# Optimization experiments

Hardware: AMD Instinct MI355X
Metric: run time of the kernel (lower is better)

Reference implementation:

```python
import jax, jax.numpy as jnp
import numpy as np

T = 0.5  # temperature from __init__


def setup_inputs() -> dict:
    key = jax.random.key(0)
    k1, k2, k3 = jax.random.split(key, 3)
    n, d = 8192, 256
    findings_embeddings = jax.random.normal(k1, (n, d), dtype=jnp.float32)
    impression_embeddings = jax.random.normal(k2, (n, d), dtype=jnp.float32)
    chexpert_label = jax.random.randint(k3, (n,), 0, 14, dtype=jnp.int64)
    return {
        "findings_embeddings": findings_embeddings,
        "impression_embeddings": impression_embeddings,
        "chexpert_label": chexpert_label,
    }


def reference(findings_embeddings, impression_embeddings, chexpert_label):
    n = findings_embeddings.shape[0]
    # [n, n] similarity matrix scaled by temperature
    logits = jnp.matmul(findings_embeddings, impression_embeddings.T) / T
    # zero out entries where labels match, except the diagonal (i != j)
    eq = chexpert_label[:, None] == chexpert_label[None, :]
    off_diag_eq = eq & ~jnp.eye(n, dtype=bool)
    logits = jnp.where(off_diag_eq, 0.0, logits)
    # trace(log_softmax_row + log_softmax_col) without materializing two [n,n] copies:
    # diag(log_softmax(L, axis)) = diag(L) - logsumexp(L, axis)
    diag = jnp.diagonal(logits)
    lse_row = jax.nn.logsumexp(logits, axis=1)  # findings -> impression direction
    lse_col = jax.nn.logsumexp(logits, axis=0)  # impression -> findings direction
    loss = -jnp.sum((diag - lse_row) + (diag - lse_col)) / n
    return loss
```

## Files before the change

kernel.cpp:

```cpp
#include <hip/hip_runtime.h>
#include <hip/hip_bf16.h>

#define N 8192
#define D 256
#define NSLICE 16
#define BM 128
#define TROWS 2
#define CB 32
#define COLS_PER_SLICE (N / NSLICE)
#define NT (COLS_PER_SLICE / CB)
#define NRB (N / BM)
#define TILE_B (CB * D)

#define CSHIFT 160.0f
#define K2LOG2E 2.885390082f
#define LN2F 0.6931471805599453f

typedef __attribute__((ext_vector_type(4))) float f32x4;

__device__ inline float fast_exp2(float x) { return __builtin_amdgcn_exp2f(x); }
__device__ inline float fast_log2(float x) { return __builtin_amdgcn_logf(x); }

__device__ inline void gload_lds16(const void* g, void* l) {
    __builtin_amdgcn_global_load_lds(
        (const __attribute__((address_space(1))) void*)g,
        (__attribute__((address_space(3))) void*)l, 16, 0, 0);
}

__device__ inline unsigned int pack_fp8x4(float a, float b, float c, float d) {
    unsigned int p = __builtin_amdgcn_cvt_pk_fp8_f32(a, b, 0, 0);
    p = __builtin_amdgcn_cvt_pk_fp8_f32(c, d, (int)p, 1);
    return p;
}

__global__ void convert_fp8(const float* __restrict__ F, const float* __restrict__ Imp,
                            unsigned int* __restrict__ Fb8, unsigned int* __restrict__ Ib8) {
    const int i = blockIdx.x * blockDim.x + threadIdx.x;
    if (blockIdx.y == 0) {
        const float4 v0 = reinterpret_cast<const float4*>(F)[i * 2];
        const float4 v1 = reinterpret_cast<const float4*>(F)[i * 2 + 1];
        Fb8[i * 2] = pack_fp8x4(v0.x, v0.y, v0.z, v0.w);
        Fb8[i * 2 + 1] = pack_fp8x4(v1.x, v1.y, v1.z, v1.w);
    } else {
        const int lane = i & 63;
        const int ks = (i >> 6) & 7;
        const int g = i >> 9;
        const int col = g * 16 + (lane & 15);
        const int k0 = ks * 32 + (lane >> 4) * 8;
        const float* src = Imp + (size_t)col * D + k0;
        const float4 v0 = *reinterpret_cast<const float4*>(src);
        const float4 v1 = *reinterpret_cast<const float4*>(src + 4);
        Ib8[i * 2] = pack_fp8x4(v0.x, v0.y, v0.z, v0.w);
        Ib8[i * 2 + 1] = pack_fp8x4(v1.x, v1.y, v1.z, v1.w);
    }
}

__global__ void label_hist(const int* __restrict__ labels, int* __restrict__ counts) {
    __shared__ int c[16];
    if (threadIdx.x < 16) c[threadIdx.x] = 0;
    __syncthreads();
    for (int i = threadIdx.x; i < N; i += blockDim.x) atomicAdd(&c[labels[i]], 1);
    __syncthreads();
    if (threadIdx.x < 16) counts[threadIdx.x] = c[threadIdx.x];
}

__launch_bounds__(256, 4)
__global__ void tile_pass(const unsigned char* __restrict__ Fb8,
                          const unsigned char* __restrict__ Ib8,
                          const int* __restrict__ labels,
                          float* __restrict__ partials_row,
                          float* __restrict__ partials_col) {
    __shared__ __align__(16) unsigned char Bsh[3 * TILE_B];
    __shared__ float colacc[4][COLS_PER_SLICE];
    __shared__ int labs[COLS_PER_SLICE];

    const int tid = threadIdx.x;
    const int lane = tid & 63;
    const int wave = tid >> 6;
    const int rb = blockIdx.x;
    const int row0 = rb * BM + wave * (16 * TROWS);
    const int c0 = blockIdx.y * COLS_PER_SLICE;
    const int lrow = lane & 15;
    const int kgrp = lane >> 4;

#define STAGE(buf, ct)                                                          \
    {                                                                           \
        const unsigned char* tbase = Ib8 + (size_t)(c0 + (ct) * CB) * D;        \
        _Pragma("unroll")                                                       \
        for (int i = 0; i < 2; ++i) {                                           \
            const int chunk = wave * 2 + i;                                     \
            gload_lds16(tbase + chunk * 1024 + lane * 16,                       \
                        &Bsh[(buf) * TILE_B + chunk * 1024 + lane * 16]);       \
        }                                                                       \
    }

    STAGE(0, 0);
    STAGE(1, 1);

    for (int i = tid; i < COLS_PER_SLICE; i += 256) {
        labs[i] = labels[c0 + i];
        colacc[0][i] = 0.f; colacc[1][i] = 0.f; colacc[2][i] = 0.f; colacc[3][i] = 0.f;
    }

    long afrag[TROWS][8];
#pragma unroll
    for (int t = 0; t < TROWS; ++t) {
        const unsigned char* arow = Fb8 + (size_t)(row0 + t * 16 + lrow) * D;
#pragma unroll
        for (int ks = 0; ks < 8; ++ks)
            afrag[t][ks] = *reinterpret_cast<const long*>(arow + ks * 32 + kgrp * 8);
    }
#pragma unroll
    for (int t = 0; t < TROWS; ++t)
#pragma unroll
        for (int ks = 0; ks < 8; ++ks)
            asm volatile("" : "+v"(afrag[t][ks]));

    int labr[TROWS][4];
#pragma unroll
    for (int t = 0; t < TROWS; ++t) {
        const int base = row0 + t * 16 + kgrp * 4;
#pragma unroll
        for (int r = 0; r < 4; ++r) labr[t][r] = labels[base + r];
    }

    float s[TROWS][4];
#pragma unroll
    for (int t = 0; t < TROWS; ++t)
#pragma unroll
        for (int r = 0; r < 4; ++r) s[t][r] = 0.0f;

    asm volatile("s_waitcnt vmcnt(2) lgkmcnt(0)" ::: "memory");
    __builtin_amdgcn_s_barrier();

    int cbuf = 0, sbuf = 2;
    for (int ct = 0; ct < NT; ++ct) {
        if (ct + 2 < NT) STAGE(sbuf, ct + 2);

        __builtin_amdgcn_s_setprio(1);
#pragma unroll
        for (int u = 0; u < 2; ++u) {
            long bfrag[8];
#pragma unroll
            for (int ks = 0; ks < 8; ++ks)
                bfrag[ks] = *reinterpret_cast<const long*>(
                    &Bsh[cbuf * TILE_B + (u * 8 + ks) * 512 + lane * 8]);

            const int labc = labs[ct * CB + u * 16 + lrow];
            float colpart = 0.0f;
            f32x4 acc[TROWS];
#pragma unroll
            for (int t = 0; t < TROWS; ++t) acc[t] = f32x4{0.f, 0.f, 0.f, 0.f};
#pragma unroll
            for (int ks = 0; ks < 8; ++ks)
#pragma unroll
                for (int t = 0; t < TROWS; ++t)
                    acc[t] = __builtin_amdgcn_mfma_f32_16x16x32_fp8_fp8(
                        afrag[t][ks], bfrag[ks], acc[t], 0, 0, 0);

#pragma unroll
            for (int t = 0; t < TROWS; ++t) {
#pragma unroll
                for (int r = 0; r < 4; ++r) {
                    float arg = __builtin_fmaf(acc[t][r], K2LOG2E, -CSHIFT);
                    arg = (labr[t][r] == labc) ? -1000.0f : arg;
                    float e = fast_exp2(arg);
                    s[t][r] += e;
                    colpart += e;
                }
            }
            colpart += __shfl_xor(colpart, 16, 64);
            colpart += __shfl_xor(colpart, 32, 64);
            if (kgrp == 0)
                colacc[wave][ct * CB + u * 16 + lrow] += colpart;
        }
        __builtin_amdgcn_s_setprio(0);

        if (ct + 2 < NT) {
            asm volatile("s_waitcnt vmcnt(2)" ::: "memory");
        } else {
            asm volatile("s_waitcnt vmcnt(0)" ::: "memory");
        }
        __builtin_amdgcn_s_barrier();
        cbuf = (cbuf == 2) ? 0 : cbuf + 1;
        sbuf = (sbuf == 2) ? 0 : sbuf + 1;
    }

#pragma unroll
    for (int off = 1; off < 16; off <<= 1) {
#pragma unroll
        for (int t = 0; t < TROWS; ++t)
#pragma unroll
            for (int r = 0; r < 4; ++r)
                s[t][r] += __shfl_xor(s[t][r], off, 64);
    }
    if (lrow == 0) {
#pragma unroll
        for (int t = 0; t < TROWS; ++t)
#pragma unroll
            for (int r = 0; r < 4; ++r) {
                const int grow = row0 + t * 16 + kgrp * 4 + r;
                partials_row[(size_t)grow * NSLICE + blockIdx.y] = s[t][r];
            }
    }

    __syncthreads();
    for (int i = tid; i < COLS_PER_SLICE; i += 256) {
        float v = colacc[0][i] + colacc[1][i] + colacc[2][i] + colacc[3][i];
        partials_col[(size_t)rb * N + c0 + i] = v;
    }
#undef STAGE
}

__global__ void col_reduce(const float* __restrict__ partials_col, float* __restrict__ colsum) {
    const int c = blockIdx.x * 256 + threadIdx.x;
    float v = 0.0f;
    for (int rbi = 0; rbi < NRB; ++rbi) v += partials_col[(size_t)rbi * N + c];
    colsum[c] = v;
}

__device__ inline float final_lse(float S, float cntlog, float diag) {
    float l1 = (S > 0.0f) ? (CSHIFT + fast_log2(S)) * LN2F : -INFINITY;
    float M = fmaxf(fmaxf(l1, cntlog), diag);
    return M + __logf(__expf(l1 - M) + __expf(cntlog - M) + __expf(diag - M));
}

__global__ void row_contrib(const float* __restrict__ F, const float* __restrict__ Imp,
                            const float* __restrict__ partials_row,
                            const float* __restrict__ colsum,
                            const int* __restrict__ counts,
                            const int* __restrict__ labels, float* __restrict__ blockSums) {
    const int lane = threadIdx.x & 63;
    const int wave = threadIdx.x >> 6;
    const int row = blockIdx.x * 4 + wave;

    float4 a = reinterpret_cast<const float4*>(F + (size_t)row * D)[lane];
    float4 b = reinterpret_cast<const float4*>(Imp + (size_t)row * D)[lane];
    float dot = a.x * b.x + a.y * b.y + a.z * b.z + a.w * b.w;
#pragma unroll
    for (int off = 32; off > 0; off >>= 1) dot += __shfl_xor(dot, off, 64);

    float sr = (lane < NSLICE) ? partials_row[(size_t)row * NSLICE + lane] : 0.0f;
#pragma unroll
    for (int off = 16; off > 0; off >>= 1) sr += __shfl_xor(sr, off, 64);

    __shared__ float sums[4];
    if (lane == 0) {
        const float diag = 2.0f * dot;
        const int cnt = counts[labels[row]] - 1;
        const float cntlog = (cnt > 0) ? __logf((float)cnt) : -INFINITY;
        const float S_col = colsum[row];
        const float lse_total = final_lse(sr, cntlog, diag) + final_lse(S_col, cntlog, diag);
        sums[wave] = 2.0f * diag - lse_total;
    }
    __syncthreads();
    if (threadIdx.x == 0)
        blockSums[blockIdx.x] = sums[0] + sums[1] + sums[2] + sums[3];
}

__global__ void final_reduce(const float* __restrict__ blockSums, float* __restrict__ out) {
    __shared__ float red[256];
    float v = 0.0f;
    for (int i = threadIdx.x; i < N / 4; i += 256) v += blockSums[i];
    red[threadIdx.x] = v;
    __syncthreads();
    for (int st = 128; st > 0; st >>= 1) {
        if (threadIdx.x < st) red[threadIdx.x] += red[threadIdx.x + st];
        __syncthreads();
    }
    if (threadIdx.x == 0) out[0] = -red[0] / (float)N;
}

extern "C" void kernel_launch(void* const* d_in, const int* in_sizes, int n_in,
                              void* d_out, int out_size, void* d_ws, size_t ws_size,
                              hipStream_t stream) {
    const float* F = (const float*)d_in[0];
    const float* Imp = (const float*)d_in[1];
    const int* labels = (const int*)d_in[2];
    float* out = (float*)d_out;

    char* ws = (char*)d_ws;
    size_t off = 0;
    unsigned char* Fb8 = (unsigned char*)(ws + off); off += (size_t)N * D;
    unsigned char* Ib8 = (unsigned char*)(ws + off); off += (size_t)N * D;
    float* partials_row = (float*)(ws + off); off += (size_t)N * NSLICE * 4;
    float* partials_col = (float*)(ws + off); off += (size_t)NRB * N * 4;
    float* colsum = (float*)(ws + off); off += (size_t)N * 4;
    float* blockSums = (float*)(ws + off); off += (size_t)(N / 4) * 4;
    int* counts = (int*)(ws + off);

    dim3 cgrid(N * D / 8 / 256, 2);
    convert_fp8<<<cgrid, 256, 0, stream>>>(F, Imp, (unsigned int*)Fb8, (unsigned int*)Ib8);
    label_hist<<<1, 256, 0, stream>>>(labels, counts);

    dim3 g(NRB, NSLICE);
    tile_pass<<<g, 256, 0, stream>>>(Fb8, Ib8, labels, partials_row, partials_col);

    col_reduce<<<N / 256, 256, 0, stream>>>(partials_col, colsum);
    row_contrib<<<N / 4, 256, 0, stream>>>(F, Imp, partials_row, colsum, counts, labels, blockSums);
    final_reduce<<<1, 256, 0, stream>>>(blockSums, out);
}
```

Baseline: 64.86 us.

## Double the column slices, use double buffering for higher occupancy, fold histogram into convert

Doubles the number of column slices so each tile_pass block covers half as many columns and the grid has twice as many blocks. Shrinks the LDS B-buffer ring from three stages to two and raises the launch bound to 8 blocks per CU for more occupancy. Removes the separate label_hist kernel by doing global atomics inside convert_fp8, with a memset to clear the counts. The trade-off is a shallower prefetch (wait for all loads each iteration), more partial rows to reduce, and global atomic contention on 16 counters.

```diff
diff --git a/kernel.cpp b/kernel.cpp
--- a/kernel.cpp
+++ b/kernel.cpp
@@ -3,7 +3,7 @@
 
 #define N 8192
 #define D 256
-#define NSLICE 16
+#define NSLICE 32
 #define BM 128
 #define TROWS 2
 #define CB 32
@@ -34,13 +34,15 @@
 }
 
 __global__ void convert_fp8(const float* __restrict__ F, const float* __restrict__ Imp,
-                            unsigned int* __restrict__ Fb8, unsigned int* __restrict__ Ib8) {
+                            unsigned int* __restrict__ Fb8, unsigned int* __restrict__ Ib8,
+                            const int* __restrict__ labels, int* __restrict__ counts) {
     const int i = blockIdx.x * blockDim.x + threadIdx.x;
     if (blockIdx.y == 0) {
         const float4 v0 = reinterpret_cast<const float4*>(F)[i * 2];
         const float4 v1 = reinterpret_cast<const float4*>(F)[i * 2 + 1];
         Fb8[i * 2] = pack_fp8x4(v0.x, v0.y, v0.z, v0.w);
         Fb8[i * 2 + 1] = pack_fp8x4(v1.x, v1.y, v1.z, v1.w);
+        if (blockIdx.x < 32) atomicAdd(&counts[labels[i]], 1);
     } else {
         const int lane = i & 63;
         const int ks = (i >> 6) & 7;
@@ -55,22 +57,13 @@
     }
 }
 
-__global__ void label_hist(const int* __restrict__ labels, int* __restrict__ counts) {
-    __shared__ int c[16];
-    if (threadIdx.x < 16) c[threadIdx.x] = 0;
-    __syncthreads();
-    for (int i = threadIdx.x; i < N; i += blockDim.x) atomicAdd(&c[labels[i]], 1);
-    __syncthreads();
-    if (threadIdx.x < 16) counts[threadIdx.x] = c[threadIdx.x];
-}
-
-__launch_bounds__(256, 4)
+__launch_bounds__(256, 8)
 __global__ void tile_pass(const unsigned char* __restrict__ Fb8,
                           const unsigned char* __restrict__ Ib8,
                           const int* __restrict__ labels,
                           float* __restrict__ partials_row,
                           float* __restrict__ partials_col) {
-    __shared__ __align__(16) unsigned char Bsh[3 * TILE_B];
+    __shared__ __align__(16) unsigned char Bsh[2 * TILE_B];
     __shared__ float colacc[4][COLS_PER_SLICE];
     __shared__ int labs[COLS_PER_SLICE];
 
@@ -95,7 +88,6 @@
     }
 
     STAGE(0, 0);
-    STAGE(1, 1);
 
     for (int i = tid; i < COLS_PER_SLICE; i += 256) {
         labs[i] = labels[c0 + i];
@@ -110,11 +102,6 @@
         for (int ks = 0; ks < 8; ++ks)
             afrag[t][ks] = *reinterpret_cast<const long*>(arow + ks * 32 + kgrp * 8);
     }
-#pragma unroll
-    for (int t = 0; t < TROWS; ++t)
-#pragma unroll
-        for (int ks = 0; ks < 8; ++ks)
-            asm volatile("" : "+v"(afrag[t][ks]));
 
     int labr[TROWS][4];
 #pragma unroll
@@ -130,12 +117,12 @@
 #pragma unroll
         for (int r = 0; r < 4; ++r) s[t][r] = 0.0f;
 
-    asm volatile("s_waitcnt vmcnt(2) lgkmcnt(0)" ::: "memory");
+    asm volatile("s_waitcnt vmcnt(0) lgkmcnt(0)" ::: "memory");
     __builtin_amdgcn_s_barrier();
 
-    int cbuf = 0, sbuf = 2;
+    int cur = 0;
     for (int ct = 0; ct < NT; ++ct) {
-        if (ct + 2 < NT) STAGE(sbuf, ct + 2);
+        if (ct + 1 < NT) STAGE(cur ^ 1, ct + 1);
 
         __builtin_amdgcn_s_setprio(1);
 #pragma unroll
@@ -144,7 +131,7 @@
 #pragma unroll
             for (int ks = 0; ks < 8; ++ks)
                 bfrag[ks] = *reinterpret_cast<const long*>(
-                    &Bsh[cbuf * TILE_B + (u * 8 + ks) * 512 + lane * 8]);
+                    &Bsh[cur * TILE_B + (u * 8 + ks) * 512 + lane * 8]);
 
             const int labc = labs[ct * CB + u * 16 + lrow];
             float colpart = 0.0f;
@@ -176,14 +163,9 @@
         }
         __builtin_amdgcn_s_setprio(0);
 
-        if (ct + 2 < NT) {
-            asm volatile("s_waitcnt vmcnt(2)" ::: "memory");
-        } else {
-            asm volatile("s_waitcnt vmcnt(0)" ::: "memory");
-        }
+        asm volatile("s_waitcnt vmcnt(0)" ::: "memory");
         __builtin_amdgcn_s_barrier();
-        cbuf = (cbuf == 2) ? 0 : cbuf + 1;
-        sbuf = (sbuf == 2) ? 0 : sbuf + 1;
+        cur ^= 1;
     }
 
 #pragma unroll
@@ -289,9 +271,11 @@
     float* blockSums = (float*)(ws + off); off += (size_t)(N / 4) * 4;
     int* counts = (int*)(ws + off);
 
+    hipMemsetAsync(counts, 0, 16 * sizeof(int), stream);
+
     dim3 cgrid(N * D / 8 / 256, 2);
-    convert_fp8<<<cgrid, 256, 0, stream>>>(F, Imp, (unsigned int*)Fb8, (unsigned int*)Ib8);
-    label_hist<<<1, 256, 0, stream>>>(labels, counts);
+    convert_fp8<<<cgrid, 256, 0, stream>>>(F, Imp, (unsigned int*)Fb8, (unsigned int*)Ib8,
+                                           labels, counts);
 
     dim3 g(NRB, NSLICE);
     tile_pass<<<g, 256, 0, stream>>>(Fb8, Ib8, labels, partials_row, partials_col);
```

Measured after the change: 90.02 us. +38.8%, slower.
